# Performance work log

Hardware: AMD Instinct MI355X
Metric: run time of the kernel (lower is better)

## Reference

```python
import jax, jax.numpy as jnp
import numpy as np

HEADS = 8
ALPHA = 0.2  # leaky relu negative slope


def setup_inputs() -> dict:
    key = jax.random.key(0)
    k1, k2, k3 = jax.random.split(key, 3)
    B, S, IN, H, F = 8, 1024, 768, HEADS, 64
    node_features = jax.random.normal(k1, (B, S, IN), dtype=jnp.float32)
    attention_mask = jnp.ones((B, S), dtype=jnp.int32)
    W = jax.random.normal(k2, (IN, H * F), dtype=jnp.float32) * 0.02
    a = jax.random.normal(k3, (2 * F,), dtype=jnp.float32) * 0.02
    return {"node_features": node_features, "attention_mask": attention_mask, "W": W, "a": a}


def reference(node_features, attention_mask, W, a):
    B, S, _ = node_features.shape
    H = HEADS
    F = W.shape[1] // H
    # Wh: [B, S, H, F]
    Wh = (node_features @ W).reshape(B, S, H, F)
    # Additive score a([Wh_i || Wh_j]) decomposes exactly into src_i + dst_j
    a_src, a_dst = a[:F], a[F:]
    src = jnp.einsum('bshf,f->bsh', Wh, a_src)  # contribution of node i
    dst = jnp.einsum('bshf,f->bsh', Wh, a_dst)  # contribution of node j
    e = src[:, :, None, :] + dst[:, None, :, :]          # [B, i, j, H]
    e = jax.nn.leaky_relu(e, negative_slope=ALPHA)
    e = jnp.transpose(e, (0, 3, 1, 2))                   # [B, H, i, j]
    mask = attention_mask[:, None, None, :] == 0         # mask over j
    e = jnp.where(mask, -jnp.inf, e)
    attn = jax.nn.softmax(e, axis=-1)                    # [B, H, S, S]
    # weighted sum over neighbors j: [B, i, H, F]
    h_prime = jnp.einsum('bhij,bjhf->bihf', attn, Wh)
    return h_prime.reshape(B, S, H * F)
```

## Files before the change

### kernel.cpp

```cpp
#include <hip/hip_runtime.h>
#include <math.h>


typedef __attribute__((ext_vector_type(8))) short short8;
typedef __attribute__((ext_vector_type(4))) float floatx4;

union Frag { short8 s8; uint4 u4; };

__device__ inline unsigned as_u(float f) { union { float f; unsigned u; } v; v.f = f; return v.u; }
__device__ inline float as_f(unsigned u) { union { unsigned u; float f; } v; v.u = u; return v.f; }

__device__ inline unsigned pk_rne(float a, float b) {
  unsigned ua = as_u(a); ua = ua + 0x7fffu + ((ua >> 16) & 1u);
  unsigned ub = as_u(b); ub = ub + 0x7fffu + ((ub >> 16) & 1u);
  return (ua >> 16) | (ub & 0xffff0000u);
}
__device__ inline unsigned short f2bf(float f) {
  unsigned u = as_u(f); u = u + 0x7fffu + ((u >> 16) & 1u);
  return (unsigned short)(u >> 16);
}

typedef __attribute__((address_space(3))) unsigned lds_u32;
typedef const __attribute__((address_space(1))) unsigned glb_u32;
__device__ inline void gload16(const void* g, void* l) {
  __builtin_amdgcn_global_load_lds((glb_u32*)g, (lds_u32*)l, 16, 0, 0);
}

__global__ __launch_bounds__(256) void prep(const float* __restrict__ W,
                                            unsigned short* __restrict__ WbT,
                                            const float* __restrict__ X,
                                            unsigned short* __restrict__ Xb) {
  int t = threadIdx.x;
  if (blockIdx.x < 96) {
    __shared__ unsigned short tile[64][72];
    int kt = blockIdx.x >> 3, nt = blockIdx.x & 7;
    int k0 = kt * 64, n0 = nt * 64;
    int kr = t >> 2, cs = (t & 3) * 16;
#pragma unroll
    for (int q = 0; q < 4; q++) {
      float4 v = *(const float4*)&W[(k0 + kr) * 512 + n0 + cs + q * 4];
      tile[cs + q * 4 + 0][kr] = f2bf(v.x);
      tile[cs + q * 4 + 1][kr] = f2bf(v.y);
      tile[cs + q * 4 + 2][kr] = f2bf(v.z);
      tile[cs + q * 4 + 3][kr] = f2bf(v.w);
    }
    __syncthreads();
    int nr = t >> 2, ks = (t & 3) * 16;
    uint4 d0 = *(const uint4*)&tile[nr][ks];
    uint4 d1 = *(const uint4*)&tile[nr][ks + 8];
    *(uint4*)&WbT[(n0 + nr) * 768 + k0 + ks] = d0;
    *(uint4*)&WbT[(n0 + nr) * 768 + k0 + ks + 8] = d1;
  } else {
    const int total = 8192 * 768 / 8;
    int stride = 512 * 256;
    for (int i = (blockIdx.x - 96) * 256 + t; i < total; i += stride) {
      float4 v0 = *(const float4*)&X[i * 8];
      float4 v1 = *(const float4*)&X[i * 8 + 4];
      uint4 o;
      o.x = pk_rne(v0.x, v0.y); o.y = pk_rne(v0.z, v0.w);
      o.z = pk_rne(v1.x, v1.y); o.w = pk_rne(v1.z, v1.w);
      *(uint4*)&Xb[i * 8] = o;
    }
  }
}

__global__ __launch_bounds__(256) void gemm_xw(const unsigned short* __restrict__ Xb,
                                               const unsigned short* __restrict__ WbT,
                                               const float* __restrict__ a,
                                               const int* __restrict__ mask,
                                               unsigned short* __restrict__ WhT,
                                               float* __restrict__ srcT,
                                               float* __restrict__ dstT) {
  __shared__ unsigned short Asm[2][128 * 64];
  __shared__ unsigned short Bsm[2][64 * 64];
  __shared__ float sd[2][128], dd[2][128];
  int t = threadIdx.x, w = t >> 6, lane = t & 63;
  int quad = lane >> 4, l15 = lane & 15;
  int m0 = blockIdx.x * 128, n0 = blockIdx.y * 64;
  int wm = (w & 1) * 64, wn = (w >> 1) * 32;

  floatx4 acc[4][2];
#pragma unroll
  for (int mt = 0; mt < 4; mt++)
#pragma unroll
    for (int nt = 0; nt < 2; nt++)
#pragma unroll
      for (int r = 0; r < 4; r++) acc[mt][nt][r] = 0.f;

  int lr = lane >> 3;
  int cb = (lane & 7) ^ lr;
  const unsigned short* pa[4];
  const unsigned short* pb[2];
#pragma unroll
  for (int i = 0; i < 4; i++)
    pa[i] = &Xb[(m0 + w * 32 + i * 8 + lr) * 768 + cb * 8];
#pragma unroll
  for (int i = 0; i < 2; i++)
    pb[i] = &WbT[(n0 + w * 16 + i * 8 + lr) * 768 + cb * 8];

#define STAGE(bsel)                                                   \
  do {                                                                \
    unsigned short* dA = &Asm[bsel][w * 2048];                        \
    unsigned short* dB = &Bsm[bsel][w * 1024];                        \
    _Pragma("unroll") for (int i = 0; i < 4; i++) {                   \
      gload16(pa[i], dA + i * 512);                                   \
      pa[i] += 64;                                                    \
    }                                                                 \
    _Pragma("unroll") for (int i = 0; i < 2; i++) {                   \
      gload16(pb[i], dB + i * 512);                                   \
      pb[i] += 64;                                                    \
    }                                                                 \
  } while (0)

  int key = l15 & 7;
  int rA[4], rB[2];
#pragma unroll
  for (int mt = 0; mt < 4; mt++) rA[mt] = (wm + mt * 16 + l15) * 64;
#pragma unroll
  for (int nt = 0; nt < 2; nt++) rB[nt] = (wn + nt * 16 + l15) * 64;

  STAGE(0);
  __syncthreads();

#pragma unroll 2
  for (int kc = 0; kc < 12; kc++) {
    const int cur = kc & 1;
    if (kc < 11) STAGE(cur ^ 1);
    const unsigned short* bufA = &Asm[cur][0];
    const unsigned short* bufB = &Bsm[cur][0];
#pragma unroll
    for (int kc2 = 0; kc2 < 2; kc2++) {
      int kb = kc2 * 4 + quad;
      int ko = (kb ^ key) * 8;
      Frag fa[4], fb[2];
#pragma unroll
      for (int mt = 0; mt < 4; mt++) fa[mt] = *(const Frag*)&bufA[rA[mt] + ko];
#pragma unroll
      for (int nt = 0; nt < 2; nt++) fb[nt] = *(const Frag*)&bufB[rB[nt] + ko];
#pragma unroll
      for (int mt = 0; mt < 4; mt++)
#pragma unroll
        for (int nt = 0; nt < 2; nt++)
          acc[mt][nt] = __builtin_amdgcn_mfma_f32_16x16x32_bf16(fa[mt].s8, fb[nt].s8,
                                                                acc[mt][nt], 0, 0, 0);
    }
    __syncthreads();
  }
#undef STAGE

  int h = n0 >> 6;
#pragma unroll
  for (int mt = 0; mt < 4; mt++) {
#pragma unroll
    for (int nt = 0; nt < 2; nt++) {
      int f = wn + nt * 16 + l15;
      int m = m0 + wm + mt * 16 + quad * 4;
      int b = m >> 10, s = m & 1023;
      floatx4 cc = acc[mt][nt];
      uint2 st;
      st.x = pk_rne(cc[0], cc[1]);
      st.y = pk_rne(cc[2], cc[3]);
      *(uint2*)&WhT[((b * 8 + h) * 64 + f) * 1024 + s] = st;
    }
  }
  {
    float asv[2] = {a[wn + l15], a[wn + 16 + l15]};
    float adv[2] = {a[64 + wn + l15], a[64 + wn + 16 + l15]};
    float psrc[4][4], pdst[4][4];
#pragma unroll
    for (int mt = 0; mt < 4; mt++)
#pragma unroll
      for (int r = 0; r < 4; r++) {
        psrc[mt][r] = acc[mt][0][r] * asv[0] + acc[mt][1][r] * asv[1];
        pdst[mt][r] = acc[mt][0][r] * adv[0] + acc[mt][1][r] * adv[1];
      }
#pragma unroll
    for (int off = 1; off < 16; off <<= 1)
#pragma unroll
      for (int mt = 0; mt < 4; mt++)
#pragma unroll
        for (int r = 0; r < 4; r++) {
          psrc[mt][r] += __shfl_xor(psrc[mt][r], off);
          pdst[mt][r] += __shfl_xor(pdst[mt][r], off);
        }
    if (l15 == 0) {
      int half = w >> 1;
#pragma unroll
      for (int mt = 0; mt < 4; mt++)
#pragma unroll
        for (int r = 0; r < 4; r++) {
          int m = wm + mt * 16 + quad * 4 + r;
          sd[half][m] = psrc[mt][r];
          dd[half][m] = pdst[mt][r];
        }
    }
    __syncthreads();
    if (t < 128) {
      int m = m0 + t;
      int b = m >> 10, s = m & 1023;
      float sv = sd[0][t] + sd[1][t];
      float dvv = dd[0][t] + dd[1][t];
      srcT[(b * 8 + h) * 1024 + s] = sv;
      dstT[(b * 8 + h) * 1024 + s] = mask[b * 1024 + s] ? dvv : -1e30f;
    }
  }
}

__global__ __launch_bounds__(256) void gat_attn(const unsigned short* __restrict__ WhT,
                                                const float* __restrict__ srcT,
                                                const float* __restrict__ dstT,
                                                float* __restrict__ out) {
  __shared__ unsigned short Bs[2][64 * 64];
  int t = threadIdx.x, w = t >> 6, lane = t & 63;
  int quad = lane >> 4, l15 = lane & 15;
  int bh = blockIdx.x, b = bh >> 3;
  int iw = blockIdx.y * 64 + w * 16;

  floatx4 acc[4], lacc;
#pragma unroll
  for (int ft = 0; ft < 4; ft++)
#pragma unroll
    for (int r = 0; r < 4; r++) acc[ft][r] = 0.f;
#pragma unroll
  for (int r = 0; r < 4; r++) lacc[r] = 0.f;

  float src_r = srcT[bh * 1024 + iw + l15];

  Frag ones;
  ones.u4.x = 0x3F803F80u; ones.u4.y = 0x3F803F80u;
  ones.u4.z = 0x3F803F80u; ones.u4.w = 0x3F803F80u;

  const unsigned short* Wg = WhT + bh * 64 * 1024;
  const float* dbase = &dstT[bh * 1024 + quad * 8];
  int sf0 = t >> 3, skb = t & 7;
  int swz = (skb ^ (sf0 & 7)) * 8;

  uint4 g0 = *(const uint4*)&Wg[sf0 * 1024 + skb * 8];
  uint4 g1 = *(const uint4*)&Wg[(sf0 + 32) * 1024 + skb * 8];
  float4 dv[4];
  dv[0] = *(const float4*)&dbase[0];
  dv[1] = *(const float4*)&dbase[4];
  dv[2] = *(const float4*)&dbase[32];
  dv[3] = *(const float4*)&dbase[36];

#pragma unroll 2
  for (int jt = 0; jt < 16; jt++) {
    int j0 = jt * 64;
    unsigned short* buf = &Bs[jt & 1][0];
    *(uint4*)&buf[sf0 * 64 + swz] = g0;
    *(uint4*)&buf[(sf0 + 32) * 64 + swz] = g1;
    __syncthreads();
    float4 ndv[4] = {dv[0], dv[1], dv[2], dv[3]};
    if (jt < 15) {
      g0 = *(const uint4*)&Wg[sf0 * 1024 + j0 + 64 + skb * 8];
      g1 = *(const uint4*)&Wg[(sf0 + 32) * 1024 + j0 + 64 + skb * 8];
      ndv[0] = *(const float4*)&dbase[j0 + 64];
      ndv[1] = *(const float4*)&dbase[j0 + 68];
      ndv[2] = *(const float4*)&dbase[j0 + 96];
      ndv[3] = *(const float4*)&dbase[j0 + 100];
    }
    Frag fragA[2];
#pragma unroll
    for (int jc = 0; jc < 2; jc++) {
      float dj[8] = {dv[jc * 2].x, dv[jc * 2].y, dv[jc * 2].z, dv[jc * 2].w,
                     dv[jc * 2 + 1].x, dv[jc * 2 + 1].y, dv[jc * 2 + 1].z, dv[jc * 2 + 1].w};
      unsigned pw[4];
#pragma unroll
      for (int pr = 0; pr < 4; pr++) {
        float x0 = src_r + dj[pr * 2];
        float x1 = src_r + dj[pr * 2 + 1];
        x0 = fmaxf(x0, 0.2f * x0);
        x1 = fmaxf(x1, 0.2f * x1);
        float p0 = __expf(x0), p1 = __expf(x1);
        pw[pr] = __builtin_amdgcn_perm(as_u(p1), as_u(p0), 0x07060302u);
      }
      fragA[jc].u4.x = pw[0];
      fragA[jc].u4.y = pw[1];
      fragA[jc].u4.z = pw[2];
      fragA[jc].u4.w = pw[3];
    }
#pragma unroll
    for (int jc = 0; jc < 2; jc++) {
      Frag fbr[4];
#pragma unroll
      for (int ft = 0; ft < 4; ft++) {
        int f = ft * 16 + l15;
        int kb = jc * 4 + quad;
        fbr[ft] = *(const Frag*)&buf[f * 64 + (kb ^ (f & 7)) * 8];
      }
#pragma unroll
      for (int ft = 0; ft < 4; ft++)
        acc[ft] = __builtin_amdgcn_mfma_f32_16x16x32_bf16(fragA[jc].s8, fbr[ft].s8,
                                                          acc[ft], 0, 0, 0);
      lacc = __builtin_amdgcn_mfma_f32_16x16x32_bf16(fragA[jc].s8, ones.s8, lacc, 0, 0, 0);
    }
#pragma unroll
    for (int q = 0; q < 4; q++) dv[q] = ndv[q];
  }
  float inv[4] = {1.f / lacc[0], 1.f / lacc[1], 1.f / lacc[2], 1.f / lacc[3]};
  int mrow = b * 1024 + iw + quad * 4;
#pragma unroll
  for (int ft = 0; ft < 4; ft++) {
    int col = (bh & 7) * 64 + ft * 16 + l15;
#pragma unroll
    for (int r = 0; r < 4; r++)
      out[(mrow + r) * 512 + col] = acc[ft][r] * inv[r];
  }
}

extern "C" void kernel_launch(void* const* d_in, const int* in_sizes, int n_in,
                              void* d_out, int out_size, void* d_ws, size_t ws_size,
                              hipStream_t stream) {
  const float* X = (const float*)d_in[0];
  const int* mask = (const int*)d_in[1];
  const float* W = (const float*)d_in[2];
  const float* a = (const float*)d_in[3];
  float* out = (float*)d_out;

  char* ws = (char*)d_ws;
  unsigned short* WhT = (unsigned short*)ws;
  unsigned short* WbT = (unsigned short*)(ws + 8388608);
  float* srcT = (float*)(ws + 9175040);
  float* dstT = (float*)(ws + 9437184);
  unsigned short* Xb = (unsigned short*)(ws + 9699328);

  prep<<<608, 256, 0, stream>>>(W, WbT, X, Xb);
  gemm_xw<<<dim3(64, 8), 256, 0, stream>>>(Xb, WbT, a, mask, WhT, srcT, dstT);
  gat_attn<<<dim3(64, 16), 256, 0, stream>>>(WhT, srcT, dstT, out);
}
```

Before: 115.0 us.

## Fuse X bf16 conversion into GEMM A-tile loading and fold log2e into scores

The separate pass that converted X to bf16 in the prep kernel is removed. The GEMM now loads fp32 X directly into registers, converts it to bf16 and writes it into swizzled LDS, software-pipelined across k-chunks. This avoids writing and re-reading the 12 MB bf16 copy of X. The cost is that the GEMM reads twice the bytes per A tile from global memory, and the conversion work plus register-staged loads now sit inside its loop. Separately, log2(e) is folded into src/dst so that attention can use the raw exp2 instruction instead of __expf.

```diff
diff --git a/kernel.cpp b/kernel.cpp
--- a/kernel.cpp
+++ b/kernel.cpp
@@ -26,45 +26,32 @@
   __builtin_amdgcn_global_load_lds((glb_u32*)g, (lds_u32*)l, 16, 0, 0);
 }
 
+#define LOG2E 1.4426950408889634f
+
 __global__ __launch_bounds__(256) void prep(const float* __restrict__ W,
-                                            unsigned short* __restrict__ WbT,
-                                            const float* __restrict__ X,
-                                            unsigned short* __restrict__ Xb) {
+                                            unsigned short* __restrict__ WbT) {
   int t = threadIdx.x;
-  if (blockIdx.x < 96) {
-    __shared__ unsigned short tile[64][72];
-    int kt = blockIdx.x >> 3, nt = blockIdx.x & 7;
-    int k0 = kt * 64, n0 = nt * 64;
-    int kr = t >> 2, cs = (t & 3) * 16;
-#pragma unroll
-    for (int q = 0; q < 4; q++) {
-      float4 v = *(const float4*)&W[(k0 + kr) * 512 + n0 + cs + q * 4];
-      tile[cs + q * 4 + 0][kr] = f2bf(v.x);
-      tile[cs + q * 4 + 1][kr] = f2bf(v.y);
-      tile[cs + q * 4 + 2][kr] = f2bf(v.z);
-      tile[cs + q * 4 + 3][kr] = f2bf(v.w);
-    }
-    __syncthreads();
-    int nr = t >> 2, ks = (t & 3) * 16;
-    uint4 d0 = *(const uint4*)&tile[nr][ks];
-    uint4 d1 = *(const uint4*)&tile[nr][ks + 8];
-    *(uint4*)&WbT[(n0 + nr) * 768 + k0 + ks] = d0;
-    *(uint4*)&WbT[(n0 + nr) * 768 + k0 + ks + 8] = d1;
-  } else {
-    const int total = 8192 * 768 / 8;
-    int stride = 512 * 256;
-    for (int i = (blockIdx.x - 96) * 256 + t; i < total; i += stride) {
-      float4 v0 = *(const float4*)&X[i * 8];
-      float4 v1 = *(const float4*)&X[i * 8 + 4];
-      uint4 o;
-      o.x = pk_rne(v0.x, v0.y); o.y = pk_rne(v0.z, v0.w);
-      o.z = pk_rne(v1.x, v1.y); o.w = pk_rne(v1.z, v1.w);
-      *(uint4*)&Xb[i * 8] = o;
-    }
-  }
-}
-
-__global__ __launch_bounds__(256) void gemm_xw(const unsigned short* __restrict__ Xb,
+  __shared__ unsigned short tile[64][72];
+  int kt = blockIdx.x >> 3, nt = blockIdx.x & 7;
+  int k0 = kt * 64, n0 = nt * 64;
+  int kr = t >> 2, cs = (t & 3) * 16;
+#pragma unroll
+  for (int q = 0; q < 4; q++) {
+    float4 v = *(const float4*)&W[(k0 + kr) * 512 + n0 + cs + q * 4];
+    tile[cs + q * 4 + 0][kr] = f2bf(v.x);
+    tile[cs + q * 4 + 1][kr] = f2bf(v.y);
+    tile[cs + q * 4 + 2][kr] = f2bf(v.z);
+    tile[cs + q * 4 + 3][kr] = f2bf(v.w);
+  }
+  __syncthreads();
+  int nr = t >> 2, ks = (t & 3) * 16;
+  uint4 d0 = *(const uint4*)&tile[nr][ks];
+  uint4 d1 = *(const uint4*)&tile[nr][ks + 8];
+  *(uint4*)&WbT[(n0 + nr) * 768 + k0 + ks] = d0;
+  *(uint4*)&WbT[(n0 + nr) * 768 + k0 + ks + 8] = d1;
+}
+
+__global__ __launch_bounds__(256) void gemm_xw(const float* __restrict__ X,
                                                const unsigned short* __restrict__ WbT,
                                                const float* __restrict__ a,
                                                const int* __restrict__ mask,
@@ -87,25 +74,22 @@
 #pragma unroll
       for (int r = 0; r < 4; r++) acc[mt][nt][r] = 0.f;
 
+  int sf0 = t >> 3, skb = t & 7;
+  int swz = (skb ^ (sf0 & 7)) * 8;
+  const float* pxa[4];
+#pragma unroll
+  for (int g = 0; g < 4; g++) pxa[g] = &X[(m0 + sf0 + 32 * g) * 768 + skb * 8];
+
   int lr = lane >> 3;
   int cb = (lane & 7) ^ lr;
-  const unsigned short* pa[4];
   const unsigned short* pb[2];
-#pragma unroll
-  for (int i = 0; i < 4; i++)
-    pa[i] = &Xb[(m0 + w * 32 + i * 8 + lr) * 768 + cb * 8];
 #pragma unroll
   for (int i = 0; i < 2; i++)
     pb[i] = &WbT[(n0 + w * 16 + i * 8 + lr) * 768 + cb * 8];
 
-#define STAGE(bsel)                                                   \
+#define STAGE_B(bsel)                                                 \
   do {                                                                \
-    unsigned short* dA = &Asm[bsel][w * 2048];                        \
     unsigned short* dB = &Bsm[bsel][w * 1024];                        \
-    _Pragma("unroll") for (int i = 0; i < 4; i++) {                   \
-      gload16(pa[i], dA + i * 512);                                   \
-      pa[i] += 64;                                                    \
-    }                                                                 \
     _Pragma("unroll") for (int i = 0; i < 2; i++) {                   \
       gload16(pb[i], dB + i * 512);                                   \
       pb[i] += 64;                                                    \
@@ -119,13 +103,34 @@
 #pragma unroll
   for (int nt = 0; nt < 2; nt++) rB[nt] = (wn + nt * 16 + l15) * 64;
 
-  STAGE(0);
+  float4 av[4][2];
+#pragma unroll
+  for (int g = 0; g < 4; g++) {
+    av[g][0] = *(const float4*)&pxa[g][0];
+    av[g][1] = *(const float4*)&pxa[g][4];
+  }
+  STAGE_B(0);
+#pragma unroll
+  for (int g = 0; g < 4; g++) {
+    uint4 o;
+    o.x = pk_rne(av[g][0].x, av[g][0].y); o.y = pk_rne(av[g][0].z, av[g][0].w);
+    o.z = pk_rne(av[g][1].x, av[g][1].y); o.w = pk_rne(av[g][1].z, av[g][1].w);
+    *(uint4*)&Asm[0][(sf0 + 32 * g) * 64 + swz] = o;
+  }
   __syncthreads();
 
 #pragma unroll 2
   for (int kc = 0; kc < 12; kc++) {
     const int cur = kc & 1;
-    if (kc < 11) STAGE(cur ^ 1);
+    if (kc < 11) {
+      STAGE_B(cur ^ 1);
+#pragma unroll
+      for (int g = 0; g < 4; g++) {
+        pxa[g] += 64;
+        av[g][0] = *(const float4*)&pxa[g][0];
+        av[g][1] = *(const float4*)&pxa[g][4];
+      }
+    }
     const unsigned short* bufA = &Asm[cur][0];
     const unsigned short* bufB = &Bsm[cur][0];
 #pragma unroll
@@ -144,9 +149,19 @@
           acc[mt][nt] = __builtin_amdgcn_mfma_f32_16x16x32_bf16(fa[mt].s8, fb[nt].s8,
                                                                 acc[mt][nt], 0, 0, 0);
     }
+    if (kc < 11) {
+      unsigned short* dA = &Asm[cur ^ 1][0];
+#pragma unroll
+      for (int g = 0; g < 4; g++) {
+        uint4 o;
+        o.x = pk_rne(av[g][0].x, av[g][0].y); o.y = pk_rne(av[g][0].z, av[g][0].w);
+        o.z = pk_rne(av[g][1].x, av[g][1].y); o.w = pk_rne(av[g][1].z, av[g][1].w);
+        *(uint4*)&dA[(sf0 + 32 * g) * 64 + swz] = o;
+      }
+    }
     __syncthreads();
   }
-#undef STAGE
+#undef STAGE_B
 
   int h = n0 >> 6;
 #pragma unroll
@@ -198,8 +213,8 @@
     if (t < 128) {
       int m = m0 + t;
       int b = m >> 10, s = m & 1023;
-      float sv = sd[0][t] + sd[1][t];
-      float dvv = dd[0][t] + dd[1][t];
+      float sv = (sd[0][t] + sd[1][t]) * LOG2E;
+      float dvv = (dd[0][t] + dd[1][t]) * LOG2E;
       srcT[(b * 8 + h) * 1024 + s] = sv;
       dstT[(b * 8 + h) * 1024 + s] = mask[b * 1024 + s] ? dvv : -1e30f;
     }
@@ -269,9 +284,8 @@
       for (int pr = 0; pr < 4; pr++) {
         float x0 = src_r + dj[pr * 2];
         float x1 = src_r + dj[pr * 2 + 1];
-        x0 = fmaxf(x0, 0.2f * x0);
-        x1 = fmaxf(x1, 0.2f * x1);
-        float p0 = __expf(x0), p1 = __expf(x1);
+        float p0 = __builtin_amdgcn_exp2f(fmaxf(x0, 0.2f * x0));
+        float p1 = __builtin_amdgcn_exp2f(fmaxf(x1, 0.2f * x1));
         pw[pr] = __builtin_amdgcn_perm(as_u(p1), as_u(p0), 0x07060302u);
       }
       fragA[jc].u4.x = pw[0];
@@ -322,9 +336,8 @@
   unsigned short* WbT = (unsigned short*)(ws + 8388608);
   float* srcT = (float*)(ws + 9175040);
   float* dstT = (float*)(ws + 9437184);
-  unsigned short* Xb = (unsigned short*)(ws + 9699328);
-
-  prep<<<608, 256, 0, stream>>>(W, WbT, X, Xb);
-  gemm_xw<<<dim3(64, 8), 256, 0, stream>>>(Xb, WbT, a, mask, WhT, srcT, dstT);
+
+  prep<<<96, 256, 0, stream>>>(W, WbT);
+  gemm_xw<<<dim3(64, 8), 256, 0, stream>>>(X, WbT, a, mask, WhT, srcT, dstT);
   gat_attn<<<dim3(64, 16), 256, 0, stream>>>(WhT, srcT, dstT, out);
 }
```

After: 116.3 us. No clear change (+1.1%).
